# Kernel optimization log

Measured on AMD Instinct MI355X. Metric: run time of the kernel, lower is better.

Reference implementation:

```python
import jax, jax.numpy as jnp
import numpy as np

D_MODEL = 1024
D_INNER = 1024
N_HEADS = 16
D_HEAD = D_INNER // N_HEADS
B = 2
CUR = 1024
PREV = 1024
LN_EPS = 1e-5


def _rel_shift(x):
    # x: (b, i, j, h) -- faithful to torch: pad along i, flat-reinterpret, drop first row
    b, i, j, h = x.shape
    zp = jnp.zeros((b, 1, j, h), x.dtype)
    xp = jnp.concatenate([zp, x], axis=1).reshape(i + 1, b, j, h)
    return xp[1:].reshape(b, i, j, h)


def setup_inputs() -> dict:
    key = jax.random.key(0)
    ks = jax.random.split(key, 10)
    x = jax.random.normal(ks[0], (B, CUR, D_MODEL), jnp.float32)
    mem = jax.random.normal(ks[1], (B, PREV, D_MODEL), jnp.float32)
    pos_emb = jax.random.normal(ks[2], (CUR + PREV, D_INNER), jnp.float32)
    u = jax.random.normal(ks[3], (N_HEADS, D_HEAD), jnp.float32) * 0.02
    v = jax.random.normal(ks[4], (N_HEADS, D_HEAD), jnp.float32) * 0.02
    # causal mask: query i (current segment) may attend key j if j <= i + PREV
    idx_i = jnp.arange(CUR)[:, None]
    idx_j = jnp.arange(CUR + PREV)[None, :]
    tgt_mask = jnp.broadcast_to((idx_j > idx_i + PREV)[None, :, :, None], (B, CUR, CUR + PREV, 1))
    Wq = jax.random.normal(ks[5], (D_INNER, D_MODEL), jnp.float32) * 0.02
    Wkv = jax.random.normal(ks[6], (2 * D_INNER, D_MODEL), jnp.float32) * 0.02
    Wfc = jax.random.normal(ks[7], (D_MODEL, D_INNER), jnp.float32) * 0.02
    bfc = jnp.zeros((D_MODEL,), jnp.float32)
    gamma = jnp.ones((D_MODEL,), jnp.float32)
    beta = jnp.zeros((D_MODEL,), jnp.float32)
    return {"x": x, "pos_emb": pos_emb, "u": u, "v": v, "mem": mem,
            "tgt_mask": tgt_mask, "Wq": Wq, "Wkv": Wkv, "Wfc": Wfc,
            "bfc": bfc, "gamma": gamma, "beta": beta}


def reference(x, pos_emb, u, v, mem, tgt_mask, Wq, Wkv, Wfc, bfc, gamma, beta):
    b, cur, _ = x.shape
    prev = mem.shape[1]
    tot = cur + prev
    h_telda = jnp.concatenate([mem, x], axis=1)               # (b, tot, d_model)
    q = jnp.einsum('bsm,im->bsi', x, Wq)                      # (b, cur, d_inner)
    kv = jnp.einsum('bsm,im->bsi', h_telda, Wkv)              # (b, tot, 2*d_inner)
    k, vv = kv[..., :D_INNER], kv[..., D_INNER:]
    q = q.reshape(b, cur, N_HEADS, D_HEAD)
    k = k.reshape(b, tot, N_HEADS, D_HEAD)
    vv = vv.reshape(b, tot, N_HEADS, D_HEAD)
    content = jnp.einsum('bihd,bjhd->bijh', q + u, k)
    pos = pos_emb.reshape(tot, N_HEADS, D_HEAD)
    pos_attn = jnp.einsum('bihd,jhd->bijh', q + v, pos)
    attn = content + _rel_shift(pos_attn)
    attn = jnp.where(tgt_mask, -jnp.inf, attn)
    attn = attn / (D_HEAD ** 0.5)
    attn = jax.nn.softmax(attn, axis=1)  # faithful: softmax over query dim as in original
    out = jnp.einsum('bijh,bjhd->bihd', attn, vv).reshape(b, cur, D_INNER)
    y = x + jnp.einsum('bsi,mi->bsm', out, Wfc) + bfc
    mu = jnp.mean(y, axis=-1, keepdims=True)
    var = jnp.mean((y - mu) ** 2, axis=-1, keepdims=True)
    return (y - mu) / jnp.sqrt(var + LN_EPS) * gamma + beta
```

## Files before the change

### kernel.cpp

```cpp
#include <hip/hip_runtime.h>
#include <hip/hip_bf16.h>
#include <stdint.h>

typedef unsigned short u16;
typedef __attribute__((ext_vector_type(8))) __bf16 bf16x8;
typedef __attribute__((ext_vector_type(4))) float f32x4;
typedef __attribute__((ext_vector_type(4))) float float4v;
typedef __attribute__((ext_vector_type(4))) u16  u16x4;

#define DEV __device__ __forceinline__

#define NB   2
#define CUR  1024
#define PREV 1024
#define TOT  2048
#define DM   1024
#define NH   16
#define DH   64

DEV u16 f2b(float f) {
    uint32_t u = __builtin_bit_cast(uint32_t, f);
    uint32_t r = (u + 0x7fffu + ((u >> 16) & 1u)) >> 16;
    return (u16)r;
}
DEV float b2f(u16 u) {
    return __builtin_bit_cast(float, (uint32_t)u << 16);
}

typedef const __attribute__((address_space(1))) void* gptr_t;
typedef __attribute__((address_space(3))) void*       lptr_t;
DEV void async16(const void* g, void* l) {
    __builtin_amdgcn_global_load_lds((gptr_t)g, (lptr_t)l, 16, 0, 0);
}

template<int BM, int BN, int BK, int WM, int WN, int EPI>
__global__ __launch_bounds__(256)
void gemm_bt(const u16* __restrict__ A, const u16* __restrict__ B,
             int M, int N, int K, long sA, long sB, int bzBase,
             void* __restrict__ C0, void* __restrict__ C1,
             const float* __restrict__ F0, const float* __restrict__ F1)
{
    constexpr int WAVES_N = BN / WN;
    constexpr int MI = WM / 16, NI = WN / 16;
    static_assert((BM / WM) * (BN / WN) == 4, "4 waves");
    static_assert(BK == 64, "swizzle assumes 8 chunks/row");

    __shared__ u16 lA[BM * BK];
    __shared__ u16 lB[BN * BK];

    const int bz = blockIdx.z;
    const int m0 = blockIdx.y * BM, n0 = blockIdx.x * BN;
    const int tid = threadIdx.x, wave = tid >> 6, lane = tid & 63;

    if constexpr (EPI == 3) {
        if (m0 > n0 + BN - 1 + PREV) return;
    }

    const u16* Ab = A + (long)bz * sA;
    const u16* Bb = B + (long)bz * sB;
    const int wm0 = (wave / WAVES_N) * WM, wn0 = (wave % WAVES_N) * WN;
    const int quad = lane >> 4;

    f32x4 acc[MI][NI];
#pragma unroll
    for (int mi = 0; mi < MI; ++mi)
#pragma unroll
        for (int ni = 0; ni < NI; ++ni)
            acc[mi][ni] = f32x4{0.f, 0.f, 0.f, 0.f};

    const int srow = tid >> 3;
    const int ksw  = (((tid & 7) ^ ((tid >> 3) & 7)) << 3);

    for (int kt = 0; kt < K; kt += BK) {
        __syncthreads();
#pragma unroll
        for (int is = 0; is < (BM * BK) / 2048; ++is) {
            int r = is * 32 + srow;
            async16(Ab + (long)(m0 + r) * K + kt + ksw, &lA[is * 2048 + wave * 512]);
        }
#pragma unroll
        for (int is = 0; is < (BN * BK) / 2048; ++is) {
            int r = is * 32 + srow;
            async16(Bb + (long)(n0 + r) * K + kt + ksw, &lB[is * 2048 + wave * 512]);
        }
        __syncthreads();
#pragma unroll
        for (int ks = 0; ks < BK; ks += 32) {
            bf16x8 af[MI], br[NI];
#pragma unroll
            for (int mi = 0; mi < MI; ++mi)
                af[mi] = *(const bf16x8*)(const void*)
                    &lA[(wm0 + mi * 16 + (lane & 15)) * BK +
                        ((((ks >> 3) + quad) ^ (lane & 7)) << 3)];
#pragma unroll
            for (int ni = 0; ni < NI; ++ni)
                br[ni] = *(const bf16x8*)(const void*)
                    &lB[(wn0 + ni * 16 + (lane & 15)) * BK +
                        ((((ks >> 3) + quad) ^ (lane & 7)) << 3)];
#pragma unroll
            for (int mi = 0; mi < MI; ++mi)
#pragma unroll
                for (int ni = 0; ni < NI; ++ni)
                    acc[mi][ni] = __builtin_amdgcn_mfma_f32_16x16x32_bf16(af[mi], br[ni], acc[mi][ni], 0, 0, 0);
        }
    }

    const int gbz = bzBase + bz;

    if constexpr (EPI == 1) {
        u16* Abuf = (u16*)C0;
        const int b = gbz;
#pragma unroll
        for (int mi = 0; mi < MI; ++mi) {
            const int m = m0 + wm0 + mi * 16 + quad * 4;
            const int h = m >> 6, d = m & 63;
            const float4v uu = *(const float4v*)(F0 + m);
            const float4v vv = *(const float4v*)(F1 + m);
#pragma unroll
            for (int ni = 0; ni < NI; ++ni) {
                const int i = n0 + wn0 + ni * 16 + (lane & 15);
                u16x4 pu, pv;
#pragma unroll
                for (int r = 0; r < 4; ++r) {
                    pu[r] = f2b(acc[mi][ni][r] + uu[r]);
                    pv[r] = f2b(acc[mi][ni][r] + vv[r]);
                }
                *(u16x4*)(Abuf + (((long)(b * NH + h)) * CUR + i) * 128 + d) = pu;
                if (b == 0) {
                    if (i > 0)
                        *(u16x4*)(Abuf + (((long)h) * CUR + (i - 1)) * 128 + 64 + d) = pv;
                    if (i == 1023) {
                        u16x4 z = {};
                        *(u16x4*)(Abuf + (((long)h) * CUR + 1023) * 128 + 64 + d) = z;
                    }
                } else {
                    *(u16x4*)(Abuf + (((long)(NH + h)) * CUR + i) * 128 + 64 + d) = pv;
                }
            }
        }
    } else if constexpr (EPI == 2) {
#pragma unroll
        for (int mi = 0; mi < MI; ++mi) {
            const int m = m0 + wm0 + mi * 16 + quad * 4;
            const bool isV = m >= DM;
            const int h = (m >> 6) & 15, d = m & 63;
#pragma unroll
            for (int ni = 0; ni < NI; ++ni) {
                const int n = n0 + wn0 + ni * 16 + (lane & 15);
                const int b = n >> 11, j = n & 2047;
                u16x4 p;
#pragma unroll
                for (int r = 0; r < 4; ++r) p[r] = f2b(acc[mi][ni][r]);
                if (!isV)
                    *(u16x4*)((u16*)C0 + (((long)(b * NH + h)) * TOT + j) * 128 + d) = p;
                else
                    *(u16x4*)((u16*)C1 + (((long)(b * NH + h)) * TOT + j) * 64 + d) = p;
            }
        }
    } else if constexpr (EPI == 3) {
        float ps[MI][4];
#pragma unroll
        for (int mi = 0; mi < MI; ++mi)
#pragma unroll
            for (int r = 0; r < 4; ++r) ps[mi][r] = 0.f;
#pragma unroll
        for (int mi = 0; mi < MI; ++mi) {
            const int m = m0 + wm0 + mi * 16 + quad * 4;
#pragma unroll
            for (int ni = 0; ni < NI; ++ni) {
                const int n = n0 + wn0 + ni * 16 + (lane & 15);
#pragma unroll
                for (int r = 0; r < 4; ++r) {
                    float e = (m + r > n + PREV) ? 0.f : __expf(acc[mi][ni][r] * 0.125f);
                    ps[mi][r] += e;
                }
            }
        }
        float* CS = (float*)C1 + (long)gbz * TOT;
#pragma unroll
        for (int mi = 0; mi < MI; ++mi)
#pragma unroll
            for (int r = 0; r < 4; ++r) {
                float vv = ps[mi][r];
                vv += __shfl_xor(vv, 1);
                vv += __shfl_xor(vv, 2);
                vv += __shfl_xor(vv, 4);
                vv += __shfl_xor(vv, 8);
                if ((lane & 15) == 0)
                    atomicAdd(CS + m0 + wm0 + mi * 16 + quad * 4 + r, vv);
            }
    } else if constexpr (EPI == 5) {
#pragma unroll
        for (int mi = 0; mi < MI; ++mi) {
            const int m = m0 + wm0 + mi * 16 + quad * 4;
            const float4v bb = *(const float4v*)(F1 + m);
#pragma unroll
            for (int ni = 0; ni < NI; ++ni) {
                const int n = n0 + wn0 + ni * 16 + (lane & 15);
                const float4v xr = *(const float4v*)(F0 + (long)n * DM + m);
                float4v y;
#pragma unroll
                for (int r = 0; r < 4; ++r) y[r] = xr[r] + acc[mi][ni][r] + bb[r];
                *(float4v*)((float*)C0 + (long)n * DM + m) = y;
            }
        }
    }
}

__global__ __launch_bounds__(256)
void fused_attn(const u16* __restrict__ Abuf, const u16* __restrict__ Bbuf,
                const u16* __restrict__ Vp, const float* __restrict__ rcs,
                u16* __restrict__ Obf)
{
    __shared__ u16 lQ[64 * 128];
    __shared__ u16 lK[64 * 128];
    __shared__ u16 lV[64 * 64];
    __shared__ u16 lP[64 * 64];

    const int bh = blockIdx.y;
    const int n0 = blockIdx.x * 64;
    const int b = bh >> 4, h = bh & 15;
    const int tid = threadIdx.x, wave = tid >> 6, lane = tid & 63;
    const int l15 = lane & 15, quad = lane >> 4;
    const int iw = wave * 16 + l15;

    const u16*  Qg = Abuf + ((long)bh * CUR + n0) * 128;
    const u16*  Kg = Bbuf + (long)bh * TOT * 128;
    const u16*  Vg = Vp + (long)bh * DH * TOT;
    const float* rc = rcs + (long)bh * TOT;

    {
        const int r = tid >> 4, c = tid & 15;
        const int cs = (c & 8) | ((c & 7) ^ (r & 7));
#pragma unroll
        for (int is = 0; is < 4; ++is)
            async16(Qg + (long)(is * 16 + r) * 128 + cs * 8, &lQ[is * 2048 + wave * 512]);
    }

    f32x4 oacc[4];
#pragma unroll
    for (int mi = 0; mi < 4; ++mi) oacc[mi] = f32x4{0.f, 0.f, 0.f, 0.f};

    const int ig = n0 + iw;
    const int nt = (n0 >> 6) + 17;

    for (int t = 0; t < nt; ++t) {
        const int j0 = t * 64;
        __syncthreads();
        {
            const int r = tid >> 4, c = tid & 15;
            const int cs = (c & 8) | ((c & 7) ^ (r & 7));
#pragma unroll
            for (int is = 0; is < 4; ++is)
                async16(Kg + (long)(j0 + is * 16 + r) * 128 + cs * 8, &lK[is * 2048 + wave * 512]);
        }
        {
            const int r = tid >> 3, c = tid & 7;
            const int cs = c ^ (r & 7);
#pragma unroll
            for (int is = 0; is < 2; ++is)
                async16(Vg + (long)(is * 32 + r) * TOT + j0 + cs * 8, &lV[is * 2048 + wave * 512]);
        }
        __syncthreads();

        f32x4 sacc[4];
#pragma unroll
        for (int smi = 0; smi < 4; ++smi) sacc[smi] = f32x4{0.f, 0.f, 0.f, 0.f};
#pragma unroll
        for (int ks = 0; ks < 128; ks += 32) {
            const int cq = (ks >> 3) + quad;
            const bf16x8 qf = *(const bf16x8*)(const void*)
                &lQ[iw * 128 + (((cq & 8) | ((cq & 7) ^ (iw & 7))) << 3)];
#pragma unroll
            for (int smi = 0; smi < 4; ++smi) {
                const int jr = smi * 16 + l15;
                const bf16x8 kf = *(const bf16x8*)(const void*)
                    &lK[jr * 128 + (((cq & 8) | ((cq & 7) ^ (jr & 7))) << 3)];
                sacc[smi] = __builtin_amdgcn_mfma_f32_16x16x32_bf16(kf, qf, sacc[smi], 0, 0, 0);
            }
        }

#pragma unroll
        for (int smi = 0; smi < 4; ++smi) {
            const int jl = smi * 16 + quad * 4;
            const int jg = j0 + jl;
            const float4v rcv = *(const float4v*)(rc + jg);
            u16x4 pk;
#pragma unroll
            for (int r = 0; r < 4; ++r) {
                float p = (jg + r > ig + PREV) ? 0.f : __expf(sacc[smi][r] * 0.125f) * rcv[r];
                pk[r] = f2b(p);
            }
            const int c16 = (jl >> 3) ^ (iw & 7);
            *(u16x4*)&lP[iw * 64 + (c16 << 3) + ((quad & 1) << 2)] = pk;
        }

#pragma unroll
        for (int ks = 0; ks < 64; ks += 32) {
            const int cp = (ks >> 3) + quad;
            const bf16x8 pb = *(const bf16x8*)(const void*)
                &lP[iw * 64 + ((cp ^ (iw & 7)) << 3)];
#pragma unroll
            for (int mi = 0; mi < 4; ++mi) {
                const int dr = mi * 16 + l15;
                const bf16x8 vf = *(const bf16x8*)(const void*)
                    &lV[dr * 64 + ((cp ^ (dr & 7)) << 3)];
                oacc[mi] = __builtin_amdgcn_mfma_f32_16x16x32_bf16(vf, pb, oacc[mi], 0, 0, 0);
            }
        }
    }

    u16* Ob = Obf + (long)b * CUR * DM + h * DH;
#pragma unroll
    for (int mi = 0; mi < 4; ++mi) {
        const int d = mi * 16 + quad * 4;
        u16x4 p;
#pragma unroll
        for (int r = 0; r < 4; ++r) p[r] = f2b(oacc[mi][r]);
        *(u16x4*)(Ob + (long)ig * DM + d) = p;
    }
}

__global__ __launch_bounds__(256)
void cvt_weights(const float* __restrict__ Wq, const float* __restrict__ Wkv,
                 const float* __restrict__ Wfc, u16* __restrict__ Wqb,
                 u16* __restrict__ Wkvb, u16* __restrict__ Wfcb)
{
    int i = blockIdx.x * 256 + threadIdx.x;
    const float* s; u16* d; int off;
    if (i < 262144)      { s = Wq;  d = Wqb;  off = i; }
    else if (i < 786432) { s = Wkv; d = Wkvb; off = i - 262144; }
    else                 { s = Wfc; d = Wfcb; off = i - 786432; }
    float4v f = ((const float4v*)s)[off];
    u16x4 o = {f2b(f[0]), f2b(f[1]), f2b(f[2]), f2b(f[3])};
    ((u16x4*)d)[off] = o;
}

__global__ __launch_bounds__(256)
void pack_H(const float* __restrict__ mem, const float* __restrict__ x, u16* __restrict__ dst)
{
    int i = blockIdx.x * 256 + threadIdx.x;
    int e = i << 2;
    int b = e >> 21, r = e & ((1 << 21) - 1);
    const float* src = (r < (1 << 20)) ? (mem + ((long)b << 20) + r)
                                       : (x + ((long)b << 20) + (r - (1 << 20)));
    float4v f = *(const float4v*)src;
    u16x4 o = {f2b(f[0]), f2b(f[1]), f2b(f[2]), f2b(f[3])};
    ((u16x4*)dst)[i] = o;
}

__global__ __launch_bounds__(256)
void pack_pos(const float* __restrict__ pos, u16* __restrict__ Bbuf)
{
    int i = blockIdx.x * 256 + threadIdx.x;
    int e = i << 2;
    int h = e >> 17, r = e & 131071, j = r >> 6, d = r & 63;
    float4v f = *(const float4v*)(pos + (long)j * DM + h * DH + d);
    u16x4 o = {f2b(f[0]), f2b(f[1]), f2b(f[2]), f2b(f[3])};
    long base = ((long)h * TOT + j) * 128 + 64 + d;
    *(u16x4*)(Bbuf + base) = o;
    *(u16x4*)(Bbuf + base + (long)NH * TOT * 128) = o;
}

__global__ __launch_bounds__(256)
void vprime_kernel(const u16* __restrict__ Vtmp, const float* __restrict__ colsum,
                   u16* __restrict__ Vp, float* __restrict__ rcs)
{
    __shared__ float t[64][65];
    int bz = blockIdx.y;
    int j0 = blockIdx.x * 64;
    const u16* src = Vtmp + ((long)bz * TOT + j0) * 64;
    const float* cs = colsum + (long)bz * TOT + j0;
    for (int e = threadIdx.x; e < 4096; e += 256) {
        int jl = e >> 6, d = e & 63;
        t[jl][d] = b2f(src[e]);
    }
    if (threadIdx.x < 64)
        rcs[(long)bz * TOT + j0 + threadIdx.x] = 1.f / cs[threadIdx.x];
    __syncthreads();
    u16* dst = Vp + (long)bz * DH * TOT + j0;
    for (int e = threadIdx.x; e < 4096; e += 256) {
        int d = e >> 6, jl = e & 63;
        dst[(long)d * TOT + jl] = f2b(t[jl][d]);
    }
}

__global__ __launch_bounds__(256)
void ln_kernel(const float* __restrict__ Y, const float* __restrict__ gamma,
               const float* __restrict__ beta, float* __restrict__ out)
{
    const int row = blockIdx.x;
    const float* y = Y + (long)row * DM;
    float v[4];
    float s = 0.f;
#pragma unroll
    for (int t = 0; t < 4; ++t) { v[t] = y[threadIdx.x + t * 256]; s += v[t]; }
#pragma unroll
    for (int off = 32; off > 0; off >>= 1) s += __shfl_down(s, off);
    __shared__ float r1[4], r2[4];
    int wv = threadIdx.x >> 6, ln = threadIdx.x & 63;
    if (ln == 0) r1[wv] = s;
    __syncthreads();
    float mu = (r1[0] + r1[1] + r1[2] + r1[3]) * (1.f / DM);
    float q = 0.f;
#pragma unroll
    for (int t = 0; t < 4; ++t) { float d = v[t] - mu; q += d * d; }
#pragma unroll
    for (int off = 32; off > 0; off >>= 1) q += __shfl_down(q, off);
    if (ln == 0) r2[wv] = q;
    __syncthreads();
    float var = (r2[0] + r2[1] + r2[2] + r2[3]) * (1.f / DM);
    float inv = rsqrtf(var + 1e-5f);
#pragma unroll
    for (int t = 0; t < 4; ++t) {
        int c = threadIdx.x + t * 256;
        out[(long)row * DM + c] = (v[t] - mu) * inv * gamma[c] + beta[c];
    }
}

extern "C" void kernel_launch(void* const* d_in, const int* in_sizes, int n_in,
                              void* d_out, int out_size, void* d_ws, size_t ws_size,
                              hipStream_t stream)
{
    const float* x     = (const float*)d_in[0];
    const float* pos   = (const float*)d_in[1];
    const float* u     = (const float*)d_in[2];
    const float* vbias = (const float*)d_in[3];
    const float* mem   = (const float*)d_in[4];
    const float* Wq    = (const float*)d_in[6];
    const float* Wkv   = (const float*)d_in[7];
    const float* Wfc   = (const float*)d_in[8];
    const float* bfc   = (const float*)d_in[9];
    const float* gamma = (const float*)d_in[10];
    const float* beta  = (const float*)d_in[11];
    float* out = (float*)d_out;

    char* w = (char*)d_ws;
    auto alloc = [&](size_t bytes) {
        char* p = w;
        w += (bytes + 255) & ~(size_t)255;
        return p;
    };
    u16*   Hb     = (u16*)alloc(4096UL * 1024 * 2);
    u16*   Wqb    = (u16*)alloc(1024UL * 1024 * 2);
    u16*   Wkvb   = (u16*)alloc(2048UL * 1024 * 2);
    u16*   Wfcb   = (u16*)alloc(1024UL * 1024 * 2);
    u16*   Abuf   = (u16*)alloc(32UL * 1024 * 128 * 2);
    u16*   Bbuf   = (u16*)alloc(32UL * 2048 * 128 * 2);
    u16*   Vtmp   = (u16*)alloc(32UL * 2048 * 64 * 2);
    u16*   Vp     = (u16*)alloc(32UL * 64 * 2048 * 2);
    float* colsum = (float*)alloc(32UL * 2048 * 4);
    float* rcs    = (float*)alloc(32UL * 2048 * 4);
    u16*   Obf    = (u16*)alloc(2048UL * 1024 * 2);
    float* Yf     = (float*)alloc(2048UL * 1024 * 4);

    hipMemsetAsync(colsum, 0, 32UL * 2048 * 4, stream);

    cvt_weights<<<4096, 256, 0, stream>>>(Wq, Wkv, Wfc, Wqb, Wkvb, Wfcb);
    pack_H  <<<4096, 256, 0, stream>>>(mem, x, Hb);
    pack_pos<<<2048, 256, 0, stream>>>(pos, Bbuf);

    gemm_bt<128, 64, 64, 64, 32, 1><<<dim3(16, 8, 2), 256, 0, stream>>>(
        Wqb, Hb + 1024UL * 1024, 1024, 1024, 1024, 0, 2048L * 1024, 0,
        Abuf, nullptr, u, vbias);
    gemm_bt<128, 128, 64, 64, 64, 2><<<dim3(32, 16, 1), 256, 0, stream>>>(
        Wkvb, Hb, 2048, 4096, 1024, 0, 0, 0, Bbuf, Vtmp, nullptr, nullptr);

    gemm_bt<128, 128, 64, 64, 64, 3><<<dim3(8, 16, 32), 256, 0, stream>>>(
        Bbuf, Abuf, 2048, 1024, 128, 2048L * 128, 1024L * 128, 0,
        nullptr, colsum, nullptr, nullptr);
    vprime_kernel<<<dim3(32, 32), 256, 0, stream>>>(Vtmp, colsum, Vp, rcs);
    fused_attn<<<dim3(16, 32), 256, 0, stream>>>(Abuf, Bbuf, Vp, rcs, Obf);

    gemm_bt<64, 128, 64, 32, 64, 5><<<dim3(16, 16, 1), 256, 0, stream>>>(
        Wfcb, Obf, 1024, 2048, 1024, 0, 0, 0, Yf, nullptr, x, bfc);
    ln_kernel<<<2048, 256, 0, stream>>>(Yf, gamma, beta, out);
}
```

Measured before the change: 215.1 us.

## Double-buffer K/V in fused attention and reuse it for column-sum pass

Replaces the separate GEMM-based column-sum kernel with a DO_PV=0 instantiation of the fused attention kernel, which computes the per-key exp sums tile by tile with one atomic per key per block. K and V tiles are double-buffered so the next tile's async loads overlap the current tile's MFMA work, removing one barrier per iteration. The grid is reordered to put heads on x and to launch the longest query tiles first, for better load balance. The cost is more LDS per block, which may reduce occupancy, and the column-sum pass now uses more atomics.

```diff
diff --git a/kernel.cpp b/kernel.cpp
--- a/kernel.cpp
+++ b/kernel.cpp
@@ -51,10 +51,6 @@
     const int bz = blockIdx.z;
     const int m0 = blockIdx.y * BM, n0 = blockIdx.x * BN;
     const int tid = threadIdx.x, wave = tid >> 6, lane = tid & 63;
-
-    if constexpr (EPI == 3) {
-        if (m0 > n0 + BN - 1 + PREV) return;
-    }
 
     const u16* Ab = A + (long)bz * sA;
     const u16* Bb = B + (long)bz * sB;
@@ -157,38 +153,6 @@
                     *(u16x4*)((u16*)C1 + (((long)(b * NH + h)) * TOT + j) * 64 + d) = p;
             }
         }
-    } else if constexpr (EPI == 3) {
-        float ps[MI][4];
-#pragma unroll
-        for (int mi = 0; mi < MI; ++mi)
-#pragma unroll
-            for (int r = 0; r < 4; ++r) ps[mi][r] = 0.f;
-#pragma unroll
-        for (int mi = 0; mi < MI; ++mi) {
-            const int m = m0 + wm0 + mi * 16 + quad * 4;
-#pragma unroll
-            for (int ni = 0; ni < NI; ++ni) {
-                const int n = n0 + wn0 + ni * 16 + (lane & 15);
-#pragma unroll
-                for (int r = 0; r < 4; ++r) {
-                    float e = (m + r > n + PREV) ? 0.f : __expf(acc[mi][ni][r] * 0.125f);
-                    ps[mi][r] += e;
-                }
-            }
-        }
-        float* CS = (float*)C1 + (long)gbz * TOT;
-#pragma unroll
-        for (int mi = 0; mi < MI; ++mi)
-#pragma unroll
-            for (int r = 0; r < 4; ++r) {
-                float vv = ps[mi][r];
-                vv += __shfl_xor(vv, 1);
-                vv += __shfl_xor(vv, 2);
-                vv += __shfl_xor(vv, 4);
-                vv += __shfl_xor(vv, 8);
-                if ((lane & 15) == 0)
-                    atomicAdd(CS + m0 + wm0 + mi * 16 + quad * 4 + r, vv);
-            }
     } else if constexpr (EPI == 5) {
 #pragma unroll
         for (int mi = 0; mi < MI; ++mi) {
@@ -207,18 +171,20 @@
     }
 }
 
+template<int DO_PV>
 __global__ __launch_bounds__(256)
 void fused_attn(const u16* __restrict__ Abuf, const u16* __restrict__ Bbuf,
                 const u16* __restrict__ Vp, const float* __restrict__ rcs,
-                u16* __restrict__ Obf)
+                float* __restrict__ colsum, u16* __restrict__ Obf)
 {
     __shared__ u16 lQ[64 * 128];
-    __shared__ u16 lK[64 * 128];
-    __shared__ u16 lV[64 * 64];
-    __shared__ u16 lP[64 * 64];
-
-    const int bh = blockIdx.y;
-    const int n0 = blockIdx.x * 64;
+    __shared__ u16 lK[2][64 * 128];
+    __shared__ u16 lV[DO_PV ? 2 * 64 * 64 : 1];
+    __shared__ u16 lP[DO_PV ? 64 * 64 : 1];
+
+    const int bh = blockIdx.x;
+    const int it = 15 - (int)blockIdx.y;
+    const int n0 = it * 64;
     const int b = bh >> 4, h = bh & 15;
     const int tid = threadIdx.x, wave = tid >> 6, lane = tid & 63;
     const int l15 = lane & 15, quad = lane >> 4;
@@ -228,96 +194,137 @@
     const u16*  Kg = Bbuf + (long)bh * TOT * 128;
     const u16*  Vg = Vp + (long)bh * DH * TOT;
     const float* rc = rcs + (long)bh * TOT;
+    float* CS = colsum + (long)bh * TOT;
+
+    const int r4 = tid >> 4, c4 = tid & 15;
+    const int csQ = ((c4 & 8) | ((c4 & 7) ^ (r4 & 7)));
+    const int r8 = tid >> 3;
+    const int csV = (tid & 7) ^ (r8 & 7);
+
+    auto stageK = [&](int t, int buf) {
+        const int j0 = t * 64;
+#pragma unroll
+        for (int is = 0; is < 4; ++is)
+            async16(Kg + (long)(j0 + is * 16 + r4) * 128 + csQ * 8,
+                    &lK[buf][is * 2048 + wave * 512]);
+    };
+    auto stageV = [&](int t, int buf) {
+        if constexpr (DO_PV) {
+            const int j0 = t * 64;
+#pragma unroll
+            for (int is = 0; is < 2; ++is)
+                async16(Vg + (long)(is * 32 + r8) * TOT + j0 + csV * 8,
+                        &lV[buf * 4096 + is * 2048 + wave * 512]);
+        }
+    };
 
     {
-        const int r = tid >> 4, c = tid & 15;
-        const int cs = (c & 8) | ((c & 7) ^ (r & 7));
 #pragma unroll
         for (int is = 0; is < 4; ++is)
-            async16(Qg + (long)(is * 16 + r) * 128 + cs * 8, &lQ[is * 2048 + wave * 512]);
-    }
+            async16(Qg + (long)(is * 16 + r4) * 128 + csQ * 8, &lQ[is * 2048 + wave * 512]);
+    }
+    stageK(0, 0);
+    stageV(0, 0);
+    __syncthreads();
 
     f32x4 oacc[4];
 #pragma unroll
     for (int mi = 0; mi < 4; ++mi) oacc[mi] = f32x4{0.f, 0.f, 0.f, 0.f};
 
     const int ig = n0 + iw;
-    const int nt = (n0 >> 6) + 17;
+    const int nt = it + 17;
 
     for (int t = 0; t < nt; ++t) {
+        const int cur = t & 1;
+        if (t + 1 < nt) { stageK(t + 1, cur ^ 1); stageV(t + 1, cur ^ 1); }
         const int j0 = t * 64;
+
+        if constexpr (DO_PV) {
+            f32x4 sacc[4];
+#pragma unroll
+            for (int smi = 0; smi < 4; ++smi) sacc[smi] = f32x4{0.f, 0.f, 0.f, 0.f};
+#pragma unroll
+            for (int ks = 0; ks < 128; ks += 32) {
+                const int cq = (ks >> 3) + quad;
+                const bf16x8 qf = *(const bf16x8*)(const void*)
+                    &lQ[iw * 128 + (((cq & 8) | ((cq & 7) ^ (iw & 7))) << 3)];
+#pragma unroll
+                for (int smi = 0; smi < 4; ++smi) {
+                    const int jr = smi * 16 + l15;
+                    const bf16x8 kf = *(const bf16x8*)(const void*)
+                        &lK[cur][jr * 128 + (((cq & 8) | ((cq & 7) ^ (jr & 7))) << 3)];
+                    sacc[smi] = __builtin_amdgcn_mfma_f32_16x16x32_bf16(kf, qf, sacc[smi], 0, 0, 0);
+                }
+            }
+#pragma unroll
+            for (int smi = 0; smi < 4; ++smi) {
+                const int jl = smi * 16 + quad * 4;
+                const int jg = j0 + jl;
+                const float4v rcv = *(const float4v*)(rc + jg);
+                u16x4 pk;
+#pragma unroll
+                for (int r = 0; r < 4; ++r) {
+                    float p = (jg + r > ig + PREV) ? 0.f : __expf(sacc[smi][r] * 0.125f) * rcv[r];
+                    pk[r] = f2b(p);
+                }
+                const int c16 = (jl >> 3) ^ (iw & 7);
+                *(u16x4*)&lP[iw * 64 + (c16 << 3) + ((quad & 1) << 2)] = pk;
+            }
+#pragma unroll
+            for (int ks = 0; ks < 64; ks += 32) {
+                const int cp = (ks >> 3) + quad;
+                const bf16x8 pb = *(const bf16x8*)(const void*)
+                    &lP[iw * 64 + ((cp ^ (iw & 7)) << 3)];
+#pragma unroll
+                for (int mi = 0; mi < 4; ++mi) {
+                    const int dr = mi * 16 + l15;
+                    const bf16x8 vf = *(const bf16x8*)(const void*)
+                        &lV[cur * 4096 + dr * 64 + ((cp ^ (dr & 7)) << 3)];
+                    oacc[mi] = __builtin_amdgcn_mfma_f32_16x16x32_bf16(vf, pb, oacc[mi], 0, 0, 0);
+                }
+            }
+        } else {
+            f32x4 sacc[4];
+#pragma unroll
+            for (int smi = 0; smi < 4; ++smi) sacc[smi] = f32x4{0.f, 0.f, 0.f, 0.f};
+#pragma unroll
+            for (int ks = 0; ks < 128; ks += 32) {
+                const int cq = (ks >> 3) + quad;
+                const bf16x8 kf = *(const bf16x8*)(const void*)
+                    &lK[cur][iw * 128 + (((cq & 8) | ((cq & 7) ^ (iw & 7))) << 3)];
+#pragma unroll
+                for (int smi = 0; smi < 4; ++smi) {
+                    const int ir = smi * 16 + l15;
+                    const bf16x8 qf = *(const bf16x8*)(const void*)
+                        &lQ[ir * 128 + (((cq & 8) | ((cq & 7) ^ (ir & 7))) << 3)];
+                    sacc[smi] = __builtin_amdgcn_mfma_f32_16x16x32_bf16(qf, kf, sacc[smi], 0, 0, 0);
+                }
+            }
+            const int jg = j0 + iw;
+            float sum = 0.f;
+#pragma unroll
+            for (int smi = 0; smi < 4; ++smi) {
+#pragma unroll
+                for (int r = 0; r < 4; ++r) {
+                    const int ii = n0 + smi * 16 + quad * 4 + r;
+                    if (jg <= ii + PREV) sum += __expf(sacc[smi][r] * 0.125f);
+                }
+            }
+            atomicAdd(CS + jg, sum);
+        }
         __syncthreads();
-        {
-            const int r = tid >> 4, c = tid & 15;
-            const int cs = (c & 8) | ((c & 7) ^ (r & 7));
-#pragma unroll
-            for (int is = 0; is < 4; ++is)
-                async16(Kg + (long)(j0 + is * 16 + r) * 128 + cs * 8, &lK[is * 2048 + wave * 512]);
-        }
-        {
-            const int r = tid >> 3, c = tid & 7;
-            const int cs = c ^ (r & 7);
-#pragma unroll
-            for (int is = 0; is < 2; ++is)
-                async16(Vg + (long)(is * 32 + r) * TOT + j0 + cs * 8, &lV[is * 2048 + wave * 512]);
-        }
-        __syncthreads();
-
-        f32x4 sacc[4];
-#pragma unroll
-        for (int smi = 0; smi < 4; ++smi) sacc[smi] = f32x4{0.f, 0.f, 0.f, 0.f};
-#pragma unroll
-        for (int ks = 0; ks < 128; ks += 32) {
-            const int cq = (ks >> 3) + quad;
-            const bf16x8 qf = *(const bf16x8*)(const void*)
-                &lQ[iw * 128 + (((cq & 8) | ((cq & 7) ^ (iw & 7))) << 3)];
-#pragma unroll
-            for (int smi = 0; smi < 4; ++smi) {
-                const int jr = smi * 16 + l15;
-                const bf16x8 kf = *(const bf16x8*)(const void*)
-                    &lK[jr * 128 + (((cq & 8) | ((cq & 7) ^ (jr & 7))) << 3)];
-                sacc[smi] = __builtin_amdgcn_mfma_f32_16x16x32_bf16(kf, qf, sacc[smi], 0, 0, 0);
-            }
-        }
-
-#pragma unroll
-        for (int smi = 0; smi < 4; ++smi) {
-            const int jl = smi * 16 + quad * 4;
-            const int jg = j0 + jl;
-            const float4v rcv = *(const float4v*)(rc + jg);
-            u16x4 pk;
-#pragma unroll
-            for (int r = 0; r < 4; ++r) {
-                float p = (jg + r > ig + PREV) ? 0.f : __expf(sacc[smi][r] * 0.125f) * rcv[r];
-                pk[r] = f2b(p);
-            }
-            const int c16 = (jl >> 3) ^ (iw & 7);
-            *(u16x4*)&lP[iw * 64 + (c16 << 3) + ((quad & 1) << 2)] = pk;
-        }
-
-#pragma unroll
-        for (int ks = 0; ks < 64; ks += 32) {
-            const int cp = (ks >> 3) + quad;
-            const bf16x8 pb = *(const bf16x8*)(const void*)
-                &lP[iw * 64 + ((cp ^ (iw & 7)) << 3)];
-#pragma unroll
-            for (int mi = 0; mi < 4; ++mi) {
-                const int dr = mi * 16 + l15;
-                const bf16x8 vf = *(const bf16x8*)(const void*)
-                    &lV[dr * 64 + ((cp ^ (dr & 7)) << 3)];
-                oacc[mi] = __builtin_amdgcn_mfma_f32_16x16x32_bf16(vf, pb, oacc[mi], 0, 0, 0);
-            }
-        }
-    }
-
-    u16* Ob = Obf + (long)b * CUR * DM + h * DH;
-#pragma unroll
-    for (int mi = 0; mi < 4; ++mi) {
-        const int d = mi * 16 + quad * 4;
-        u16x4 p;
-#pragma unroll
-        for (int r = 0; r < 4; ++r) p[r] = f2b(oacc[mi][r]);
-        *(u16x4*)(Ob + (long)ig * DM + d) = p;
+    }
+
+    if constexpr (DO_PV) {
+        u16* Ob = Obf + (long)b * CUR * DM + h * DH;
+#pragma unroll
+        for (int mi = 0; mi < 4; ++mi) {
+            const int d = mi * 16 + quad * 4;
+            u16x4 p;
+#pragma unroll
+            for (int r = 0; r < 4; ++r) p[r] = f2b(oacc[mi][r]);
+            *(u16x4*)(Ob + (long)ig * DM + d) = p;
+        }
     }
 }
 
@@ -466,11 +473,11 @@
     gemm_bt<128, 128, 64, 64, 64, 2><<<dim3(32, 16, 1), 256, 0, stream>>>(
         Wkvb, Hb, 2048, 4096, 1024, 0, 0, 0, Bbuf, Vtmp, nullptr, nullptr);
 
-    gemm_bt<128, 128, 64, 64, 64, 3><<<dim3(8, 16, 32), 256, 0, stream>>>(
-        Bbuf, Abuf, 2048, 1024, 128, 2048L * 128, 1024L * 128, 0,
-        nullptr, colsum, nullptr, nullptr);
+    fused_attn<0><<<dim3(32, 16), 256, 0, stream>>>(
+        Abuf, Bbuf, nullptr, nullptr, colsum, nullptr);
     vprime_kernel<<<dim3(32, 32), 256, 0, stream>>>(Vtmp, colsum, Vp, rcs);
-    fused_attn<<<dim3(16, 32), 256, 0, stream>>>(Abuf, Bbuf, Vp, rcs, Obf);
+    fused_attn<1><<<dim3(32, 16), 256, 0, stream>>>(
+        Abuf, Bbuf, Vp, rcs, nullptr, Obf);
 
     gemm_bt<64, 128, 64, 32, 64, 5><<<dim3(16, 16, 1), 256, 0, stream>>>(
         Wfcb, Obf, 1024, 2048, 1024, 0, 0, 0, Yf, nullptr, x, bfc);
```

Result: slower. 283.3 us (+31.7%).
